# Performance work log

Hardware: AMD Instinct MI355X
Metric: run time of the kernel (lower is better)

The kernel has to match this reference:

```python
import jax, jax.numpy as jnp
import numpy as np

TOPK = 3
RAT_S = 0.05


def _zero_window_mask(h, w, rat_s=RAT_S):
    # mask[src_pixel, tgt_r, tgt_c] = 1 - gauss_r * gauss_c, gaussian centered at src pixel
    sr = h * rat_s
    sc = w * rat_s
    rows = jnp.arange(h, dtype=jnp.float32)
    cols = jnp.arange(w, dtype=jnp.float32)
    gr = jnp.exp(-((rows[None, :] - rows[:, None]) ** 2) / (2.0 * sr * sr))  # (h_src, h_tgt)
    gc = jnp.exp(-((cols[None, :] - cols[:, None]) ** 2) / (2.0 * sc * sc))  # (w_src, w_tgt)
    mask = 1.0 - gr[:, None, :, None] * gc[None, :, None, :]                 # (h,w,h,w)
    return mask.reshape(h * w, h * w)


def setup_inputs() -> dict:
    key = jax.random.key(0)
    b, c, h, w = 2, 256, 64, 64
    x = jax.random.normal(key, (b, c, h, w), dtype=jnp.float32)
    alpha = jnp.float32(5.0)
    return {"x": x, "alpha": alpha}


def reference(x, alpha):
    b, c, h, w = x.shape
    hw = h * w
    # L2-normalize over channels (F.normalize eps=1e-12 uses max(norm, eps))
    nrm = jnp.sqrt(jnp.sum(x * x, axis=1, keepdims=True))
    xn = x / jnp.maximum(nrm, 1e-12)
    xf = xn.reshape(b, c, hw)
    # (b, hw_src, hw_tgt) affinity
    aff = jnp.einsum('bcs,bct->bst', xf, xf)
    mask = _zero_window_mask(h, w)
    x_aff = aff * mask[None]                               # (b, hw, hw)
    logits = x_aff * alpha
    x_c = jax.nn.softmax(logits, axis=-1) * jax.nn.softmax(logits, axis=-2)
    xc_o = x_c.reshape(b, hw, h, w)
    # top-k over source-pixel axis (dim=-3)
    val = jax.lax.top_k(jnp.moveaxis(xc_o, 1, -1), TOPK)[0]  # (b,h,w,k)
    val = jnp.moveaxis(val, -1, 1)                           # (b,k,h,w)
    x_soft = xc_o / (jnp.sum(xc_o, axis=1, keepdims=True) + 1e-8)
    return (val, x_soft)
```

## Files before the change

kernel.cpp:

```cpp
#include <hip/hip_runtime.h>

#define HW 4096
#define CDIM 256
#define BK 32

typedef _Float16 half8 __attribute__((ext_vector_type(8)));
typedef float f32x4 __attribute__((ext_vector_type(4)));

__device__ __forceinline__ void top3_ins(float v, float& a0, float& a1, float& a2) {
  float m01 = fminf(a0, v);
  a0 = fmaxf(a0, v);
  float m12 = fminf(a1, m01);
  a1 = fmaxf(a1, m01);
  a2 = fmaxf(a2, m12);
}

__device__ __forceinline__ float mask_val(const float* gtab, int s, int t) {
  int dr = (s >> 6) - (t >> 6); dr = dr < 0 ? -dr : dr;
  int dc = (s & 63) - (t & 63); dc = dc < 0 ? -dc : dc;
  return 1.0f - gtab[dr] * gtab[dc];
}

__device__ __forceinline__ void async_copy16(const void* g, void* l) {
  __builtin_amdgcn_global_load_lds((const __attribute__((address_space(1))) void*)g,
                                   (__attribute__((address_space(3))) void*)l, 16, 0, 0);
}

__device__ __forceinline__ void stage_slice(const _Float16* __restrict__ X,
                                            int rowBase, int k0,
                                            _Float16* sdst, int w, int lane) {
  const int csrc = ((lane & 3) - ((lane >> 3) & 3)) & 3;
#pragma unroll
  for (int i = 0; i < 2; ++i) {
    const int rchunk = w * 32 + i * 16;
    const _Float16* g =
        X + (size_t)(rowBase + rchunk + (lane >> 2)) * CDIM + k0 + csrc * 8;
    async_copy16(g, sdst + rchunk * BK);
  }
}

__global__ void __launch_bounds__(256) normalize_k(const float* __restrict__ x,
                                                   _Float16* __restrict__ Xf) {
  const int p = threadIdx.x & 31;
  const int g = threadIdx.x >> 5;
  const int P0 = blockIdx.x * 32;
  const int b = P0 >> 12;
  const int ph = (P0 & (HW - 1)) + p;
  const float* xb = x + (size_t)b * CDIM * HW + ph;
  float vals[32];
  float ss = 0.f;
#pragma unroll
  for (int k = 0; k < 32; ++k) {
    float v = xb[(size_t)(g * 32 + k) * HW];
    vals[k] = v;
    ss += v * v;
  }
  __shared__ float ssqp[8][33];
  __shared__ float scl[32];
  ssqp[g][p] = ss;
  __syncthreads();
  if (threadIdx.x < 32) {
    float s2 = 0.f;
#pragma unroll
    for (int gg = 0; gg < 8; ++gg) s2 += ssqp[gg][threadIdx.x];
    scl[threadIdx.x] = 1.0f / fmaxf(sqrtf(s2), 1e-12f);
  }
  __syncthreads();
  const float sc = scl[p];
  _Float16* o = Xf + (size_t)(P0 + p) * CDIM + g * 32;
#pragma unroll
  for (int c8 = 0; c8 < 4; ++c8) {
    half8 h;
#pragma unroll
    for (int j = 0; j < 8; ++j) h[j] = (_Float16)(vals[c8 * 8 + j] * sc);
    *(half8*)(o + c8 * 8) = h;
  }
}

__global__ void __launch_bounds__(256, 3) gemmE16_k(const _Float16* __restrict__ Xf,
                                                    const float* __restrict__ alphap,
                                                    float* __restrict__ R,
                                                    float* __restrict__ outX) {
  __shared__ _Float16 smem[4][128 * BK];
  __shared__ float gtab[64];
  if (threadIdx.x < 64) {
    float d = (float)threadIdx.x;
    gtab[threadIdx.x] = __expf(-d * d * 0.048828125f);
  }
  const float alpha = alphap[0];
  const int b = blockIdx.z;
  const _Float16* X = Xf + (size_t)b * HW * CDIM;
  const int lane = threadIdx.x & 63;
  const int w = threadIdx.x >> 6;
  const int wr = w >> 1, wc = w & 1;
  const int mBase = blockIdx.y * 128;
  const int nBase = blockIdx.x * 128;

  f32x4 acc[4][4];
#pragma unroll
  for (int mi = 0; mi < 4; ++mi)
#pragma unroll
    for (int ni = 0; ni < 4; ++ni) acc[mi][ni] = (f32x4){0.f, 0.f, 0.f, 0.f};

  const int aRow0 = wr * 64 + (lane & 15);
  const int bRow0 = wc * 64 + (lane & 15);
  const int cswz = (((lane >> 4) + ((lane >> 1) & 3)) & 3) * 8;

  stage_slice(X, mBase, 0, smem[0], w, lane);
  stage_slice(X, nBase, 0, smem[2], w, lane);

  int cur = 0;
#pragma unroll
  for (int k0 = 0; k0 < CDIM; k0 += BK) {
    __syncthreads();
    if (k0 + BK < CDIM) {
      stage_slice(X, mBase, k0 + BK, smem[cur ^ 1], w, lane);
      stage_slice(X, nBase, k0 + BK, smem[2 + (cur ^ 1)], w, lane);
    }
    half8 a[4], bfr[4];
#pragma unroll
    for (int i = 0; i < 4; ++i)
      a[i] = *(const half8*)(smem[cur] + (aRow0 + 16 * i) * BK + cswz);
#pragma unroll
    for (int i = 0; i < 4; ++i)
      bfr[i] = *(const half8*)(smem[2 + cur] + (bRow0 + 16 * i) * BK + cswz);
#pragma unroll
    for (int mi = 0; mi < 4; ++mi)
#pragma unroll
      for (int ni = 0; ni < 4; ++ni)
        acc[mi][ni] = __builtin_amdgcn_mfma_f32_16x16x32_f16(a[mi], bfr[ni], acc[mi][ni], 0, 0, 0);
    cur ^= 1;
  }

  __syncthreads();
  _Float16* et = &smem[0][0];
  const int quad = lane >> 4;
  float csum[4] = {0.f, 0.f, 0.f, 0.f};
#pragma unroll
  for (int mi = 0; mi < 4; ++mi) {
#pragma unroll
    for (int r = 0; r < 4; ++r) {
      const int row = wr * 64 + mi * 16 + quad * 4 + r;
      const int s = mBase + row;
      const int v = (row >> 2) & 7;
#pragma unroll
      for (int ni = 0; ni < 4; ++ni) {
        const int col = wc * 64 + ni * 16 + (lane & 15);
        const int t = nBase + col;
        float e = __expf(alpha * mask_val(gtab, s, t) * acc[mi][ni][r]);
        csum[ni] += e;
        et[row * 128 + ((((col >> 4) ^ v) << 4) | (col & 15))] = (_Float16)e;
      }
    }
  }
#pragma unroll
  for (int off = 16; off < 64; off <<= 1)
#pragma unroll
    for (int ni = 0; ni < 4; ++ni) csum[ni] += __shfl_xor(csum[ni], off);
  if (quad == 0) {
#pragma unroll
    for (int ni = 0; ni < 4; ++ni)
      atomicAdd(&R[b * HW + nBase + wc * 64 + ni * 16 + (lane & 15)], csum[ni]);
  }
  __syncthreads();
  _Float16* Hb = (_Float16*)(outX + (size_t)b * HW * HW);
  const int c8 = threadIdx.x & 15;
  const int r0 = threadIdx.x >> 4;
#pragma unroll
  for (int pass = 0; pass < 8; ++pass) {
    const int row = pass * 16 + r0;
    const int v = (row >> 2) & 7;
    half8 hv = *(const half8*)(et + row * 128 + ((((c8 >> 1) ^ v) << 4) | ((c8 & 1) * 8)));
    *(half8*)(Hb + (size_t)(mBase + row) * (2 * HW) + nBase + c8 * 8) = hv;
  }
}

__global__ void __launch_bounds__(256) colstats16_k(const float* __restrict__ outX,
                                                    const float* __restrict__ R,
                                                    float* __restrict__ T,
                                                    float* __restrict__ part) {
  const int b = blockIdx.z;
  const _Float16* Hb = (const _Float16*)(outX + (size_t)b * HW * HW);
  const float* Rb = R + b * HW;
  const int s0 = blockIdx.x * 1024;
  const int t0 = blockIdx.y * 64;
  const int tg = threadIdx.x & 7;
  const int sr = threadIdx.x >> 3;
  float ts[8], q0[8], q1[8], q2[8];
#pragma unroll
  for (int j = 0; j < 8; ++j) { ts[j] = 0.f; q0[j] = 0.f; q1[j] = 0.f; q2[j] = 0.f; }
#pragma unroll 4
  for (int k = 0; k < 32; ++k) {
    const int s = s0 + k * 32 + sr;
    const float inv = 1.0f / Rb[s];
    half8 ev = *(const half8*)(Hb + (size_t)s * (2 * HW) + t0 + tg * 8);
#pragma unroll
    for (int j = 0; j < 8; ++j) {
      float e = (float)ev[j];
      float gval = e * e * inv;
      ts[j] += gval;
      top3_ins(gval, q0[j], q1[j], q2[j]);
    }
  }
  __shared__ float Tp[32][68], P0a[32][68], P1a[32][68], P2a[32][68];
#pragma unroll
  for (int j = 0; j < 8; ++j) {
    Tp[sr][tg * 8 + j] = ts[j];
    P0a[sr][tg * 8 + j] = q0[j];
    P1a[sr][tg * 8 + j] = q1[j];
    P2a[sr][tg * 8 + j] = q2[j];
  }
  __syncthreads();
  if (threadIdx.x < 64) {
    float tsum = 0.f, a0 = 0.f, a1 = 0.f, a2 = 0.f;
#pragma unroll
    for (int s2 = 0; s2 < 32; ++s2) {
      tsum += Tp[s2][threadIdx.x];
      top3_ins(P0a[s2][threadIdx.x], a0, a1, a2);
      top3_ins(P1a[s2][threadIdx.x], a0, a1, a2);
      top3_ins(P2a[s2][threadIdx.x], a0, a1, a2);
    }
    const int t = t0 + threadIdx.x;
    atomicAdd(&T[b * HW + t], tsum);
    float* pp = part + ((size_t)(b * 4 + blockIdx.x) * HW + t) * 3;
    pp[0] = a0;
    pp[1] = a1;
    pp[2] = a2;
  }
}

__global__ void __launch_bounds__(256) merge_k(const float* __restrict__ R,
                                               const float* __restrict__ T,
                                               const float* __restrict__ part,
                                               float* __restrict__ W,
                                               float* __restrict__ val_out) {
  const int idx = blockIdx.x * 256 + threadIdx.x;
  const int b = idx >> 12;
  const int t = idx & (HW - 1);
  float a0 = 0.f, a1 = 0.f, a2 = 0.f;
#pragma unroll
  for (int c = 0; c < 4; ++c) {
    const float* pp = part + ((size_t)(b * 4 + c) * HW + t) * 3;
    top3_ins(pp[0], a0, a1, a2);
    top3_ins(pp[1], a0, a1, a2);
    top3_ins(pp[2], a0, a1, a2);
  }
  const float r = R[idx];
  const float invr = 1.0f / r;
  val_out[(b * 3 + 0) * HW + t] = a0 * invr;
  val_out[(b * 3 + 1) * HW + t] = a1 * invr;
  val_out[(b * 3 + 2) * HW + t] = a2 * invr;
  W[idx] = 1.0f / (T[idx] + 1e-8f * r);
}

#define WROWS 8
typedef _Float16 half4v __attribute__((ext_vector_type(4)));
__global__ void __launch_bounds__(256) writeout16_k(const float* __restrict__ R,
                                                    const float* __restrict__ W,
                                                    float* __restrict__ X) {
  const int b = blockIdx.y;
  float* Xb = X + (size_t)b * HW * HW;
  const _Float16* Hb = (const _Float16*)Xb;
  const float* Wb = W + b * HW;
  const float* Rb = R + b * HW;
  const int s0 = blockIdx.x * WROWS;
  f32x4 wv[4];
#pragma unroll
  for (int it = 0; it < 4; ++it)
    wv[it] = *(const f32x4*)(Wb + it * 1024 + threadIdx.x * 4);
  half4v ehA[4], ehB[4];
#pragma unroll
  for (int it = 0; it < 4; ++it)
    ehA[it] = *(const half4v*)(Hb + (size_t)s0 * (2 * HW) + it * 1024 + threadIdx.x * 4);
#pragma unroll
  for (int row = 0; row < WROWS; ++row) {
    __syncthreads();
    if (row + 1 < WROWS) {
      const _Float16* hn = Hb + (size_t)(s0 + row + 1) * (2 * HW);
#pragma unroll
      for (int it = 0; it < 4; ++it) {
        half4v v = *(const half4v*)(hn + it * 1024 + threadIdx.x * 4);
        if (row & 1) ehA[it] = v; else ehB[it] = v;
      }
    }
    const float inv = 1.0f / Rb[s0 + row];
    float* rowp = Xb + (size_t)(s0 + row) * HW;
#pragma unroll
    for (int it = 0; it < 4; ++it) {
      const int t = it * 1024 + threadIdx.x * 4;
      half4v cur = (row & 1) ? ehB[it] : ehA[it];
      f32x4 o;
#pragma unroll
      for (int j = 0; j < 4; ++j) {
        float e = (float)cur[j];
        o[j] = e * e * inv * wv[it][j];
      }
      *(f32x4*)(rowp + t) = o;
    }
  }
}

extern "C" void kernel_launch(void* const* d_in, const int* in_sizes, int n_in,
                              void* d_out, int out_size, void* d_ws, size_t ws_size,
                              hipStream_t stream) {
  const float* x = (const float*)d_in[0];
  const float* alphap = (const float*)d_in[1];
  float* out = (float*)d_out;
  float* out_val = out;
  float* out_x = out + 2 * 3 * HW;
  char* ws = (char*)d_ws;

  _Float16* Xf = (_Float16*)ws;
  float* R = (float*)(ws + (size_t)4194304);
  float* T = R + 2 * HW;
  float* W = T + 2 * HW;
  float* part = W + 2 * HW;

  hipMemsetAsync(R, 0, (size_t)2 * HW * 2 * sizeof(float), stream);

  normalize_k<<<dim3(256), dim3(256), 0, stream>>>(x, Xf);
  gemmE16_k<<<dim3(32, 32, 2), dim3(256), 0, stream>>>(Xf, alphap, R, out_x);
  colstats16_k<<<dim3(4, 64, 2), dim3(256), 0, stream>>>(out_x, R, T, part);
  merge_k<<<dim3(32), dim3(256), 0, stream>>>(R, T, part, W, out_val);
  writeout16_k<<<dim3(512, 2), dim3(256), 0, stream>>>(R, W, out_x);
}
```

Measured before the change: 204.6 us.

## Exploit affinity symmetry by computing only upper-triangular GEMM tiles

The affinity matrix and mask are symmetric, so the GEMM+exp kernel now launches only the 528 upper-triangular 128x128 tiles per batch instead of all 1024. Each off-diagonal tile also writes its transposed exp tile through shared memory and adds row sums to R via atomics alongside the column sums. This roughly halves MFMA work and exp evaluation. The cost is extra register pressure from saving the fp16 values, an extra LDS transpose pass with two barriers, and more atomics.

```diff
diff --git a/kernel.cpp b/kernel.cpp
--- a/kernel.cpp
+++ b/kernel.cpp
@@ -5,6 +5,7 @@
 #define BK 32
 
 typedef _Float16 half8 __attribute__((ext_vector_type(8)));
+typedef _Float16 half4v __attribute__((ext_vector_type(4)));
 typedef float f32x4 __attribute__((ext_vector_type(4)));
 
 __device__ __forceinline__ void top3_ins(float v, float& a0, float& a1, float& a2) {
@@ -19,6 +20,14 @@
   int dr = (s >> 6) - (t >> 6); dr = dr < 0 ? -dr : dr;
   int dc = (s & 63) - (t & 63); dc = dc < 0 ? -dc : dc;
   return 1.0f - gtab[dr] * gtab[dc];
+}
+
+__device__ __forceinline__ void tri_map(int L, int& i, int& j) {
+  int jj = (int)((sqrtf(8.f * (float)L + 1.f) - 1.f) * 0.5f);
+  while ((jj + 1) * (jj + 2) / 2 <= L) ++jj;
+  while (jj * (jj + 1) / 2 > L) --jj;
+  j = jj;
+  i = L - jj * (jj + 1) / 2;
 }
 
 __device__ __forceinline__ void async_copy16(const void* g, void* l) {
@@ -87,14 +96,17 @@
     float d = (float)threadIdx.x;
     gtab[threadIdx.x] = __expf(-d * d * 0.048828125f);
   }
+  int iT, jT;
+  tri_map(blockIdx.x, iT, jT);
+  const int mBase = iT * 128;
+  const int nBase = jT * 128;
+  const bool offd = (iT != jT);
   const float alpha = alphap[0];
   const int b = blockIdx.z;
   const _Float16* X = Xf + (size_t)b * HW * CDIM;
   const int lane = threadIdx.x & 63;
   const int w = threadIdx.x >> 6;
   const int wr = w >> 1, wc = w & 1;
-  const int mBase = blockIdx.y * 128;
-  const int nBase = blockIdx.x * 128;
 
   f32x4 acc[4][4];
 #pragma unroll
@@ -135,6 +147,8 @@
   __syncthreads();
   _Float16* et = &smem[0][0];
   const int quad = lane >> 4;
+  float* Rb = R + b * HW;
+  half4v esave[4][4];
   float csum[4] = {0.f, 0.f, 0.f, 0.f};
 #pragma unroll
   for (int mi = 0; mi < 4; ++mi) {
@@ -143,13 +157,22 @@
       const int row = wr * 64 + mi * 16 + quad * 4 + r;
       const int s = mBase + row;
       const int v = (row >> 2) & 7;
+      float rsum = 0.f;
 #pragma unroll
       for (int ni = 0; ni < 4; ++ni) {
         const int col = wc * 64 + ni * 16 + (lane & 15);
         const int t = nBase + col;
         float e = __expf(alpha * mask_val(gtab, s, t) * acc[mi][ni][r]);
         csum[ni] += e;
-        et[row * 128 + ((((col >> 4) ^ v) << 4) | (col & 15))] = (_Float16)e;
+        rsum += e;
+        _Float16 eh = (_Float16)e;
+        esave[mi][r][ni] = eh;
+        et[row * 128 + ((((col >> 4) ^ v) << 4) | (col & 15))] = eh;
+      }
+      if (offd) {
+#pragma unroll
+        for (int off = 1; off < 16; off <<= 1) rsum += __shfl_xor(rsum, off);
+        if ((lane & 15) == 0) atomicAdd(&Rb[s], rsum);
       }
     }
   }
@@ -160,7 +183,7 @@
   if (quad == 0) {
 #pragma unroll
     for (int ni = 0; ni < 4; ++ni)
-      atomicAdd(&R[b * HW + nBase + wc * 64 + ni * 16 + (lane & 15)], csum[ni]);
+      atomicAdd(&Rb[nBase + wc * 64 + ni * 16 + (lane & 15)], csum[ni]);
   }
   __syncthreads();
   _Float16* Hb = (_Float16*)(outX + (size_t)b * HW * HW);
@@ -172,6 +195,30 @@
     const int v = (row >> 2) & 7;
     half8 hv = *(const half8*)(et + row * 128 + ((((c8 >> 1) ^ v) << 4) | ((c8 & 1) * 8)));
     *(half8*)(Hb + (size_t)(mBase + row) * (2 * HW) + nBase + c8 * 8) = hv;
+  }
+  if (offd) {
+    __syncthreads();
+#pragma unroll
+    for (int mi = 0; mi < 4; ++mi) {
+#pragma unroll
+      for (int r = 0; r < 4; ++r) {
+        const int row = wr * 64 + mi * 16 + quad * 4 + r;
+#pragma unroll
+        for (int ni = 0; ni < 4; ++ni) {
+          const int col = wc * 64 + ni * 16 + (lane & 15);
+          et[col * 128 + ((((row >> 4) ^ ((col >> 2) & 7)) << 4) | (row & 15))] =
+              esave[mi][r][ni];
+        }
+      }
+    }
+    __syncthreads();
+#pragma unroll
+    for (int pass = 0; pass < 8; ++pass) {
+      const int tl = pass * 16 + r0;
+      const int v2 = (tl >> 2) & 7;
+      half8 hv = *(const half8*)(et + tl * 128 + ((((c8 >> 1) ^ v2) << 4) | ((c8 & 1) * 8)));
+      *(half8*)(Hb + (size_t)(nBase + tl) * (2 * HW) + mBase + c8 * 8) = hv;
+    }
   }
 }
 
@@ -254,7 +301,6 @@
 }
 
 #define WROWS 8
-typedef _Float16 half4v __attribute__((ext_vector_type(4)));
 __global__ void __launch_bounds__(256) writeout16_k(const float* __restrict__ R,
                                                     const float* __restrict__ W,
                                                     float* __restrict__ X) {
@@ -319,7 +365,7 @@
   hipMemsetAsync(R, 0, (size_t)2 * HW * 2 * sizeof(float), stream);
 
   normalize_k<<<dim3(256), dim3(256), 0, stream>>>(x, Xf);
-  gemmE16_k<<<dim3(32, 32, 2), dim3(256), 0, stream>>>(Xf, alphap, R, out_x);
+  gemmE16_k<<<dim3(528, 1, 2), dim3(256), 0, stream>>>(Xf, alphap, R, out_x);
   colstats16_k<<<dim3(4, 64, 2), dim3(256), 0, stream>>>(out_x, R, T, part);
   merge_k<<<dim3(32), dim3(256), 0, stream>>>(R, T, part, W, out_val);
   writeout16_k<<<dim3(512, 2), dim3(256), 0, stream>>>(R, W, out_x);
```

Result: no change. 207.0 us (+1.2%).
